# Kernel tuning notes

Measured on AMD Instinct MI355X. Metric: run time of the kernel, lower is better.

## Reference

```python
import jax, jax.numpy as jnp
import numpy as np

N, E = 50000, 800000
NODE_DIM, EDGE_DIM, TIME_DIM, OUT_DIM, N_HEADS = 128, 64, 16, 128, 4
IN_DIM = NODE_DIM + EDGE_DIM + TIME_DIM  # msg_proj input


def setup_inputs() -> dict:
    key = jax.random.key(0)
    ks = jax.random.split(key, 8)
    x = jax.random.normal(ks[0], (N, NODE_DIM), dtype=jnp.float32)
    edge_index = jax.random.randint(ks[1], (2, E), 0, N, dtype=jnp.int32)
    edge_feat = jax.random.normal(ks[2], (E, EDGE_DIM), dtype=jnp.float32)
    time_deltas = jax.random.uniform(ks[3], (E,), dtype=jnp.float32)
    # parameters
    gammas = jnp.ones((TIME_DIM,), jnp.float32)  # ExponentialTimeDecay init_gamma=1.0
    Wm = 0.02 * jax.random.normal(ks[4], (IN_DIM, OUT_DIM), dtype=jnp.float32)
    bm = jnp.zeros((OUT_DIM,), jnp.float32)
    Wa = 0.02 * jax.random.normal(ks[5], (2 * OUT_DIM, N_HEADS), dtype=jnp.float32)
    ba = jnp.zeros((N_HEADS,), jnp.float32)
    Wo = 0.02 * jax.random.normal(ks[6], (OUT_DIM + NODE_DIM, OUT_DIM), dtype=jnp.float32)
    bo = jnp.zeros((OUT_DIM,), jnp.float32)
    ln_g = jnp.ones((OUT_DIM,), jnp.float32)
    ln_b = jnp.zeros((OUT_DIM,), jnp.float32)
    return {"x": x, "edge_index": edge_index, "edge_feat": edge_feat,
            "time_deltas": time_deltas, "gammas": gammas, "Wm": Wm, "bm": bm,
            "Wa": Wa, "ba": ba, "Wo": Wo, "bo": bo, "ln_g": ln_g, "ln_b": ln_b}


def reference(x, edge_index, edge_feat, time_deltas, gammas, Wm, bm, Wa, ba, Wo, bo, ln_g, ln_b):
    src, dst = edge_index[0], edge_index[1]
    # exponential time decay encoding: (E, TIME_DIM)
    dt = jnp.clip(time_deltas, 0.0)[:, None]
    time_enc = jnp.exp(-jax.nn.softplus(gammas)[None, :] * dt)
    # gather + project messages: (E, OUT_DIM)
    msg_in = jnp.concatenate([x[src], edge_feat, time_enc], axis=-1)
    msgs = msg_in @ Wm + bm
    # edge attention, softmax over ALL edges (dim=0, as in the torch code)
    attn_in = jnp.concatenate([msgs, x[dst]], axis=-1)  # (E, 2*OUT_DIM)
    attn_logits = attn_in @ Wa + ba                      # (E, N_HEADS)
    attn_weight = jnp.mean(jax.nn.softmax(attn_logits, axis=0), axis=-1, keepdims=True)
    weighted = msgs * attn_weight
    # scatter-add into per-node aggregates: (N, OUT_DIM)
    agg = jax.ops.segment_sum(weighted, dst, num_segments=N)
    # output MLP (dropout is identity in eval) + LayerNorm
    out = jax.nn.gelu(jnp.concatenate([agg, x], axis=-1) @ Wo + bo, approximate=False)
    mu = jnp.mean(out, axis=-1, keepdims=True)
    var = jnp.mean((out - mu) ** 2, axis=-1, keepdims=True)
    return (out - mu) / jnp.sqrt(var + 1e-5) * ln_g + ln_b
```

## Files before the change

kernel.cpp:

```cpp
#include <hip/hip_runtime.h>
#include <math.h>

#define N_NODES 50000
#define N_EDGES 800000
#define ND 128
#define ED 64
#define TD 16
#define OD 128
#define NH 4
#define INDIM 208
#define K2DIM 336
#define KPAD 352
#define WTPITCH 360
#define NPAD 50048

#define OFF_A      0ll
#define OFF_EINFO  8808448ll
#define OFF_RANK   12008448ll
#define OFF_DENOM  12808448ll
#define OFF_SPG    12808464ll
#define OFF_WFUSE  12808480ll
#define OFF_BFUSE  12809312ll
#define OFF_BMO    12809328ll
#define OFF_XS4    12809456ll
#define OFF_XD4    13009456ll
#define OFF_CNT    13209456ll
#define OFF_START  13259456ll
#define OFF_SW     13309472ll
#define OFF_WT     13359520ll
#define OFF_EFC    13382560ll
#define OFF_XBF    38982560ll
#define WS_FLOATS  42182560ll

typedef __attribute__((ext_vector_type(8))) short short8v;
typedef __attribute__((ext_vector_type(4))) float f32x4;

__device__ inline unsigned short f2bf(float f) {
  unsigned u = __float_as_uint(f);
  unsigned r = (u + 0x7fffu + ((u >> 16) & 1u)) >> 16;
  return (unsigned short)r;
}
__device__ inline float bf2f(unsigned us) {
  return __uint_as_float(us << 16);
}

__global__ void k0_prep(const float* __restrict__ Wm, const float* __restrict__ bm,
                        const float* __restrict__ Wa, const float* __restrict__ ba,
                        const float* __restrict__ Wo, const float* __restrict__ gammas,
                        float* __restrict__ ws) {
  int b = blockIdx.x, j = threadIdx.x;
  unsigned short* Wt = (unsigned short*)(ws + OFF_WT);
  if (b < INDIM) {
    float acc = 0.f;
    for (int m = 0; m < OD; ++m) acc += Wm[b * OD + m] * Wo[m * OD + j];
    Wt[j * WTPITCH + b] = f2bf(acc);
    if (j < NH) {
      float a = 0.f;
      for (int m = 0; m < OD; ++m) a += Wm[b * OD + m] * Wa[m * NH + j];
      ws[OFF_WFUSE + (long)b * NH + j] = a;
    }
  } else if (b < K2DIM) {
    Wt[j * WTPITCH + b] = f2bf(Wo[(OD + b - INDIM) * OD + j]);
  } else {
    if (j < TD) ws[OFF_SPG + j] = log1pf(expf(gammas[j]));
    if (j < NH) {
      float a = ba[j];
      for (int m = 0; m < OD; ++m) a += bm[m] * Wa[m * NH + j];
      ws[OFF_BFUSE + j] = a;
    }
    float a2 = 0.f;
    for (int m = 0; m < OD; ++m) a2 += bm[m] * Wo[m * OD + j];
    ws[OFF_BMO + j] = a2;
    for (int p = K2DIM; p < KPAD; ++p) Wt[j * WTPITCH + p] = 0;
  }
}

__global__ __launch_bounds__(256) void k0b_nodeproj(
    const float* __restrict__ x, const float* __restrict__ Wa,
    float* __restrict__ ws) {
  __shared__ float wf[ND * NH];
  __shared__ float wab[ND * NH];
  int tid = threadIdx.x;
  for (int i = tid; i < ND * NH; i += 256) { wf[i] = ws[OFF_WFUSE + i]; wab[i] = Wa[ND * NH + i]; }
  __syncthreads();
  int lane = tid & 63, wv = tid >> 6;
  long n = (long)blockIdx.x * 4 + wv;
  if (n >= N_NODES) return;
  float v0 = x[n * ND + lane], v1 = x[n * ND + 64 + lane];
  unsigned short* xbf = (unsigned short*)(ws + OFF_XBF);
  xbf[n * ND + lane] = f2bf(v0);
  xbf[n * ND + 64 + lane] = f2bf(v1);
  float s0, s1, s2, s3, d0, d1, d2, d3;
  s0 = v0 * wf[lane * 4 + 0] + v1 * wf[(64 + lane) * 4 + 0];
  s1 = v0 * wf[lane * 4 + 1] + v1 * wf[(64 + lane) * 4 + 1];
  s2 = v0 * wf[lane * 4 + 2] + v1 * wf[(64 + lane) * 4 + 2];
  s3 = v0 * wf[lane * 4 + 3] + v1 * wf[(64 + lane) * 4 + 3];
  d0 = v0 * wab[lane * 4 + 0] + v1 * wab[(64 + lane) * 4 + 0];
  d1 = v0 * wab[lane * 4 + 1] + v1 * wab[(64 + lane) * 4 + 1];
  d2 = v0 * wab[lane * 4 + 2] + v1 * wab[(64 + lane) * 4 + 2];
  d3 = v0 * wab[lane * 4 + 3] + v1 * wab[(64 + lane) * 4 + 3];
  for (int off = 32; off; off >>= 1) {
    s0 += __shfl_xor(s0, off); s1 += __shfl_xor(s1, off);
    s2 += __shfl_xor(s2, off); s3 += __shfl_xor(s3, off);
    d0 += __shfl_xor(d0, off); d1 += __shfl_xor(d1, off);
    d2 += __shfl_xor(d2, off); d3 += __shfl_xor(d3, off);
  }
  if (lane == 0) {
    reinterpret_cast<float4*>(ws + OFF_XS4)[n] = make_float4(s0, s1, s2, s3);
    reinterpret_cast<float4*>(ws + OFF_XD4)[n] = make_float4(d0, d1, d2, d3);
  }
}

__global__ __launch_bounds__(256) void k_count(const int* __restrict__ ei,
                                               float* __restrict__ ws) {
  int* cnt = reinterpret_cast<int*>(ws + OFF_CNT);
  int* rank = reinterpret_cast<int*>(ws + OFF_RANK);
  for (long e = (long)blockIdx.x * 256 + threadIdx.x; e < N_EDGES;
       e += (long)gridDim.x * 256)
    rank[e] = atomicAdd(&cnt[ei[N_EDGES + e]], 1);
}

__global__ __launch_bounds__(1024) void k_scan(float* __restrict__ ws) {
  const int* cnt = reinterpret_cast<const int*>(ws + OFF_CNT);
  int* startp = reinterpret_cast<int*>(ws + OFF_START);
  __shared__ int wsum[16];
  int tid = threadIdx.x;
  int lo = tid * 49, hi = min(lo + 49, N_NODES);
  int s = 0;
  for (int i = lo; i < hi; ++i) s += cnt[i];
  int lane = tid & 63, wv = tid >> 6;
  int sc = s;
  for (int off = 1; off < 64; off <<= 1) {
    int t = __shfl_up(sc, off);
    if (lane >= off) sc += t;
  }
  if (lane == 63) wsum[wv] = sc;
  __syncthreads();
  if (tid == 0) {
    int run = 0;
    for (int i = 0; i < 16; ++i) { int t = wsum[i]; wsum[i] = run; run += t; }
  }
  __syncthreads();
  int run = wsum[wv] + sc - s;
  for (int i = lo; i < hi; ++i) { startp[i] = run; run += cnt[i]; }
  if (tid == 1023) startp[N_NODES] = run;
}

__global__ __launch_bounds__(256) void k1c(
    const int* __restrict__ ei, const float* __restrict__ ef,
    const float* __restrict__ td, float* __restrict__ ws) {
  __shared__ float wef[ED * NH];
  __shared__ float wte[TD * NH];
  __shared__ float bf[NH];
  __shared__ float spg[TD];
  __shared__ float part[NH];
  int tid = threadIdx.x;
  for (int i = tid; i < ED * NH; i += 256) wef[i] = ws[OFF_WFUSE + ND * NH + i];
  if (tid < TD * NH) wte[tid] = ws[OFF_WFUSE + (ND + ED) * NH + tid];
  if (tid < NH) { bf[tid] = ws[OFF_BFUSE + tid]; part[tid] = 0.f; }
  if (tid < TD) spg[tid] = ws[OFF_SPG + tid];
  __syncthreads();

  int lane = tid & 63;
  int q = lane >> 4, r = lane & 15, h = r & 3;
  long wid = ((long)blockIdx.x * 256 + tid) >> 6;
  long stride = (long)gridDim.x * 16;
  const float4* ef4 = reinterpret_cast<const float4*>(ef);
  const float* xsf = ws + OFF_XS4;
  const float* xdf = ws + OFF_XD4;
  const int* rank = reinterpret_cast<const int*>(ws + OFF_RANK);
  const int* startp = reinterpret_cast<const int*>(ws + OFF_START);
  uint2* efc2 = reinterpret_cast<uint2*>(ws + OFF_EFC);
  uint4* einfoC = reinterpret_cast<uint4*>(ws + OFF_EINFO);

  float wr[16];
#pragma unroll
  for (int i = 0; i < 16; ++i) wr[i] = wef[16 * r + i];
  float spg_r = spg[r];
  float wt0 = wte[r * 4 + 0], wt1 = wte[r * 4 + 1];
  float wt2 = wte[r * 4 + 2], wt3 = wte[r * 4 + 3];
  float bfh = bf[h];
  float p = 0.f;
  int base16 = lane & 48;

  for (long e = wid * 4 + q; e < N_EDGES; e += stride) {
    int s = ei[e];
    int d = ei[N_EDGES + e];
    float dt = fmaxf(td[e], 0.f);
    int pos = startp[d] + rank[e];
    float4 efv = ef4[e * 16 + r];
    float ls = xsf[4l * s + h];
    float ld = xdf[4l * d + h];
    float te = __expf(-spg_r * dt);
    uint2 eb;
    eb.x = (unsigned)f2bf(efv.x) | ((unsigned)f2bf(efv.y) << 16);
    eb.y = (unsigned)f2bf(efv.z) | ((unsigned)f2bf(efv.w) << 16);
    efc2[(long)pos * 16 + r] = eb;
    float a0 = efv.x * wr[0] + efv.y * wr[4] + efv.z * wr[8]  + efv.w * wr[12] + te * wt0;
    float a1 = efv.x * wr[1] + efv.y * wr[5] + efv.z * wr[9]  + efv.w * wr[13] + te * wt1;
    float a2 = efv.x * wr[2] + efv.y * wr[6] + efv.z * wr[10] + efv.w * wr[14] + te * wt2;
    float a3 = efv.x * wr[3] + efv.y * wr[7] + efv.z * wr[11] + efv.w * wr[15] + te * wt3;
    a0 += __shfl_xor(a0, 1); a1 += __shfl_xor(a1, 1);
    a2 += __shfl_xor(a2, 1); a3 += __shfl_xor(a3, 1);
    a0 += __shfl_xor(a0, 2); a1 += __shfl_xor(a1, 2);
    a2 += __shfl_xor(a2, 2); a3 += __shfl_xor(a3, 2);
    float v = a0;
    v = (h == 1) ? a1 : v;
    v = (h == 2) ? a2 : v;
    v = (h == 3) ? a3 : v;
    v += __shfl_xor(v, 4);
    v += __shfl_xor(v, 8);
    float ev = __expf(v + ls + ld + bfh);
    if (r < 4) p += ev;
    float e0 = __shfl(ev, base16 + 0), e1 = __shfl(ev, base16 + 1);
    float e2 = __shfl(ev, base16 + 2), e3 = __shfl(ev, base16 + 3);
    if (r == 0) {
      unsigned dt16 = (unsigned)(dt * 65535.f + 0.5f);
      if (dt16 > 65535u) dt16 = 65535u;
      uint4 pk;
      pk.x = (unsigned)s | (dt16 << 16);
      pk.y = (unsigned)f2bf(e0) | ((unsigned)f2bf(e1) << 16);
      pk.z = (unsigned)f2bf(e2) | ((unsigned)f2bf(e3) << 16);
      pk.w = 0u;
      einfoC[pos] = pk;
    }
  }
  p += __shfl_xor(p, 16);
  p += __shfl_xor(p, 32);
  if (lane < 4) atomicAdd(&part[lane], p);
  __syncthreads();
  if (tid < NH) atomicAdd(&ws[OFF_DENOM + tid], part[tid]);
}

__global__ __launch_bounds__(256) void k4a_agg(float* __restrict__ ws) {
  __shared__ float spg_s[TD];
  __shared__ float invs[NH];
  int tid = threadIdx.x;
  if (tid < TD) spg_s[tid] = ws[OFF_SPG + tid];
  if (tid < NH) invs[tid] = 0.25f / ws[OFF_DENOM + tid];
  __syncthreads();
  int lane = tid & 63;
  long wid = (long)blockIdx.x * 4 + (tid >> 6);
  long nw = (long)gridDim.x * 4;
  const int* start = reinterpret_cast<const int*>(ws + OFF_START);
  const uint4* einfoC = reinterpret_cast<const uint4*>(ws + OFF_EINFO);
  unsigned short* A = (unsigned short*)(ws + OFF_A);
  const unsigned short* xbf = (const unsigned short*)(ws + OFF_XBF);
  const unsigned short* efc = (const unsigned short*)(ws + OFF_EFC);
  float spg_l = spg_s[lane & 15];
  float inv0 = invs[0], inv1 = invs[1], inv2 = invs[2], inv3 = invs[3];

  for (long n = wid; n < N_NODES; n += nw) {
    int i0 = start[n], i1 = start[n + 1];
    float a0 = 0.f, a1 = 0.f, a2 = 0.f, a3 = 0.f, asw = 0.f;
    for (int base = i0; base < i1; base += 64) {
      int m = min(64, i1 - base);
      uint4 pk = make_uint4(0u, 0u, 0u, 0u);
      if (lane < m) pk = einfoC[base + lane];
      int j = 0;
      for (; j + 4 <= m; j += 4) {
        unsigned xu[4], zu[4], wu[4];
#pragma unroll
        for (int u = 0; u < 4; ++u) {
          xu[u] = (unsigned)__shfl((int)pk.x, j + u);
          zu[u] = (unsigned)__shfl((int)pk.y, j + u);
          wu[u] = (unsigned)__shfl((int)pk.z, j + u);
        }
        unsigned xa[4], xb[4], ec[4];
#pragma unroll
        for (int u = 0; u < 4; ++u) {
          int s = (int)(xu[u] & 0xffffu);
          xa[u] = xbf[(long)s * ND + lane];
          xb[u] = xbf[(long)s * ND + 64 + lane];
          ec[u] = efc[(long)(base + j + u) * ED + lane];
        }
#pragma unroll
        for (int u = 0; u < 4; ++u) {
          float w = bf2f(zu[u] & 0xffffu) * inv0 + bf2f(zu[u] >> 16) * inv1 +
                    bf2f(wu[u] & 0xffffu) * inv2 + bf2f(wu[u] >> 16) * inv3;
          float dt = (float)(xu[u] >> 16) * (1.f / 65535.f);
          a0 += w * bf2f(xa[u]);
          a1 += w * bf2f(xb[u]);
          a2 += w * bf2f(ec[u]);
          a3 += w * __expf(-spg_l * dt);
          asw += w;
        }
      }
      for (; j < m; ++j) {
        unsigned xu = (unsigned)__shfl((int)pk.x, j);
        unsigned zu = (unsigned)__shfl((int)pk.y, j);
        unsigned wu = (unsigned)__shfl((int)pk.z, j);
        int s = (int)(xu & 0xffffu);
        float w = bf2f(zu & 0xffffu) * inv0 + bf2f(zu >> 16) * inv1 +
                  bf2f(wu & 0xffffu) * inv2 + bf2f(wu >> 16) * inv3;
        float dt = (float)(xu >> 16) * (1.f / 65535.f);
        a0 += w * bf2f(xbf[(long)s * ND + lane]);
        a1 += w * bf2f(xbf[(long)s * ND + 64 + lane]);
        a2 += w * bf2f(efc[(long)(base + j) * ED + lane]);
        a3 += w * __expf(-spg_l * dt);
        asw += w;
      }
    }
    unsigned short* Ar = A + n * KPAD;
    Ar[lane] = f2bf(a0);
    Ar[64 + lane] = f2bf(a1);
    Ar[128 + lane] = f2bf(a2);
    if (lane < TD) Ar[192 + lane] = f2bf(a3);
    Ar[INDIM + lane] = xbf[n * ND + lane];
    Ar[INDIM + 64 + lane] = xbf[n * ND + 64 + lane];
    if (lane < 16) Ar[K2DIM + lane] = 0;
    if (lane == 0) ws[OFF_SW + n] = asw;
  }
}

__global__ __launch_bounds__(256) void k4b_mlp(
    const float* __restrict__ bo, const float* __restrict__ lng,
    const float* __restrict__ lnb, const float* __restrict__ ws,
    float* __restrict__ out) {
  __shared__ unsigned short wt[128 * WTPITCH];
  __shared__ float tbl[512];
  int tid = threadIdx.x;
  {
    const unsigned* wg = (const unsigned*)(ws + OFF_WT);
    unsigned* wl = (unsigned*)wt;
    for (int i = tid; i < 128 * WTPITCH / 2; i += 256) wl[i] = wg[i];
    if (tid < 128) {
      tbl[tid] = bo[tid];
      tbl[128 + tid] = ws[OFF_BMO + tid];
      tbl[256 + tid] = lng[tid];
      tbl[384 + tid] = lnb[tid];
    }
  }
  __syncthreads();

  int lane = tid & 63, wv = tid >> 6;
  int c0 = lane & 15, grp = lane >> 4;
  long n0 = (long)blockIdx.x * 64 + (long)wv * 16;
  const unsigned short* A = (const unsigned short*)(ws + OFF_A);
  const unsigned short* Arow = A + (n0 + c0) * KPAD;

  f32x4 acc[8];
#pragma unroll
  for (int t = 0; t < 8; ++t) acc[t] = (f32x4){0.f, 0.f, 0.f, 0.f};

#pragma unroll
  for (int kt = 0; kt < 11; ++kt) {
    short8v afrag = *reinterpret_cast<const short8v*>(Arow + kt * 32 + grp * 8);
#pragma unroll
    for (int t = 0; t < 8; ++t) {
      short8v bfrag = *reinterpret_cast<const short8v*>(&wt[(t * 16 + c0) * WTPITCH + kt * 32 + grp * 8]);
      acc[t] = __builtin_amdgcn_mfma_f32_16x16x32_bf16(afrag, bfrag, acc[t], 0, 0, 0);
    }
  }

  const float* swp = ws + OFF_SW;
  float res[4][8];
#pragma unroll
  for (int r = 0; r < 4; ++r) {
    long row = n0 + grp * 4 + r;
    float sw = swp[row];
    float s = 0.f, s2 = 0.f;
#pragma unroll
    for (int t = 0; t < 8; ++t) {
      int col = c0 + 16 * t;
      float a = acc[t][r] + tbl[col] + sw * tbl[128 + col];
      float h = 0.5f * a * (1.f + erff(a * 0.70710678118654752f));
      res[r][t] = h;
      s += h; s2 += h * h;
    }
    s += __shfl_xor(s, 1);  s2 += __shfl_xor(s2, 1);
    s += __shfl_xor(s, 2);  s2 += __shfl_xor(s2, 2);
    s += __shfl_xor(s, 4);  s2 += __shfl_xor(s2, 4);
    s += __shfl_xor(s, 8);  s2 += __shfl_xor(s2, 8);
    float mu = s * (1.f / 128.f);
    float var = s2 * (1.f / 128.f) - mu * mu;
    float rstd = rsqrtf(var + 1e-5f);
    if (row < N_NODES) {
      float* op = out + row * OD;
#pragma unroll
      for (int t = 0; t < 8; ++t) {
        int col = c0 + 16 * t;
        op[col] = (res[r][t] - mu) * rstd * tbl[256 + col] + tbl[384 + col];
      }
    }
  }
}

extern "C" void kernel_launch(void* const* d_in, const int* in_sizes, int n_in,
                              void* d_out, int out_size, void* d_ws, size_t ws_size,
                              hipStream_t stream) {
  const float* x   = (const float*)d_in[0];
  const int*   ei  = (const int*)d_in[1];
  const float* ef  = (const float*)d_in[2];
  const float* td  = (const float*)d_in[3];
  const float* gm  = (const float*)d_in[4];
  const float* Wm  = (const float*)d_in[5];
  const float* bm  = (const float*)d_in[6];
  const float* Wa  = (const float*)d_in[7];
  const float* ba  = (const float*)d_in[8];
  const float* Wo  = (const float*)d_in[9];
  const float* bo  = (const float*)d_in[10];
  const float* lng = (const float*)d_in[11];
  const float* lnb = (const float*)d_in[12];
  float* ws = (float*)d_ws;
  float* out = (float*)d_out;
  if (ws_size < (size_t)WS_FLOATS * 4) return;

  hipMemsetAsync(ws + OFF_CNT, 0, 50000 * 4, stream);
  hipMemsetAsync(ws + OFF_DENOM, 0, 64, stream);

  k0_prep<<<K2DIM + 1, 128, 0, stream>>>(Wm, bm, Wa, ba, Wo, gm, ws);
  k0b_nodeproj<<<12500, 256, 0, stream>>>(x, Wa, ws);
  k_count<<<2048, 256, 0, stream>>>(ei, ws);
  k_scan<<<1, 1024, 0, stream>>>(ws);
  k1c<<<2048, 256, 0, stream>>>(ei, ef, td, ws);
  k4a_agg<<<2048, 256, 0, stream>>>(ws);
  k4b_mlp<<<(NPAD / 64), 256, 0, stream>>>(bo, lng, lnb, ws, out);
}
```

Before: 412.8 us.

## Remap edge-logit lanes per head and stage edge info in LDS

In the edge pass, each lane now computes a 16-feature partial dot product for a single head, which removes most of the cross-lane shuffle reduction and the per-head select. The bf16 edge-feature copy is now written with wider 16-byte stores by one lane per group. The packed edge-info record is reorganised so that each of four lanes writes its own 32-bit word holding one head's exp value, with the source index and quantised dt packed into the upper halves. The aggregation kernel stages each 64-edge chunk of these records in per-wave LDS and reads them back as uint4, replacing the broadcast shuffles. The trade-off is redundant float4 loads across the four head lanes and four exps per lane instead of one.

```diff
diff --git a/kernel.cpp b/kernel.cpp
--- a/kernel.cpp
+++ b/kernel.cpp
@@ -152,17 +152,17 @@
   __shared__ float wef[ED * NH];
   __shared__ float wte[TD * NH];
   __shared__ float bf[NH];
-  __shared__ float spg[TD];
+  __shared__ float spgs[TD];
   __shared__ float part[NH];
   int tid = threadIdx.x;
   for (int i = tid; i < ED * NH; i += 256) wef[i] = ws[OFF_WFUSE + ND * NH + i];
   if (tid < TD * NH) wte[tid] = ws[OFF_WFUSE + (ND + ED) * NH + tid];
   if (tid < NH) { bf[tid] = ws[OFF_BFUSE + tid]; part[tid] = 0.f; }
-  if (tid < TD) spg[tid] = ws[OFF_SPG + tid];
+  if (tid < TD) spgs[tid] = ws[OFF_SPG + tid];
   __syncthreads();
 
   int lane = tid & 63;
-  int q = lane >> 4, r = lane & 15, h = r & 3;
+  int q = lane >> 4, r = lane & 15, h = r & 3, c = r >> 2;
   long wid = ((long)blockIdx.x * 256 + tid) >> 6;
   long stride = (long)gridDim.x * 16;
   const float4* ef4 = reinterpret_cast<const float4*>(ef);
@@ -170,59 +170,59 @@
   const float* xdf = ws + OFF_XD4;
   const int* rank = reinterpret_cast<const int*>(ws + OFF_RANK);
   const int* startp = reinterpret_cast<const int*>(ws + OFF_START);
-  uint2* efc2 = reinterpret_cast<uint2*>(ws + OFF_EFC);
-  uint4* einfoC = reinterpret_cast<uint4*>(ws + OFF_EINFO);
-
-  float wr[16];
-#pragma unroll
-  for (int i = 0; i < 16; ++i) wr[i] = wef[16 * r + i];
-  float spg_r = spg[r];
-  float wt0 = wte[r * 4 + 0], wt1 = wte[r * 4 + 1];
-  float wt2 = wte[r * 4 + 2], wt3 = wte[r * 4 + 3];
+  uint4* efc4 = reinterpret_cast<uint4*>(ws + OFF_EFC);
+  unsigned* einfoU = reinterpret_cast<unsigned*>(ws + OFF_EINFO);
+
+  float wk[16];
+#pragma unroll
+  for (int i = 0; i < 16; ++i) wk[i] = wef[(16 * c + i) * 4 + h];
+  float wt4[4], sp4[4];
+#pragma unroll
+  for (int i = 0; i < 4; ++i) { wt4[i] = wte[(4 * c + i) * 4 + h]; sp4[i] = spgs[4 * c + i]; }
   float bfh = bf[h];
   float p = 0.f;
-  int base16 = lane & 48;
 
   for (long e = wid * 4 + q; e < N_EDGES; e += stride) {
     int s = ei[e];
     int d = ei[N_EDGES + e];
     float dt = fmaxf(td[e], 0.f);
     int pos = startp[d] + rank[e];
-    float4 efv = ef4[e * 16 + r];
-    float ls = xsf[4l * s + h];
-    float ld = xdf[4l * d + h];
-    float te = __expf(-spg_r * dt);
-    uint2 eb;
-    eb.x = (unsigned)f2bf(efv.x) | ((unsigned)f2bf(efv.y) << 16);
-    eb.y = (unsigned)f2bf(efv.z) | ((unsigned)f2bf(efv.w) << 16);
-    efc2[(long)pos * 16 + r] = eb;
-    float a0 = efv.x * wr[0] + efv.y * wr[4] + efv.z * wr[8]  + efv.w * wr[12] + te * wt0;
-    float a1 = efv.x * wr[1] + efv.y * wr[5] + efv.z * wr[9]  + efv.w * wr[13] + te * wt1;
-    float a2 = efv.x * wr[2] + efv.y * wr[6] + efv.z * wr[10] + efv.w * wr[14] + te * wt2;
-    float a3 = efv.x * wr[3] + efv.y * wr[7] + efv.z * wr[11] + efv.w * wr[15] + te * wt3;
-    a0 += __shfl_xor(a0, 1); a1 += __shfl_xor(a1, 1);
-    a2 += __shfl_xor(a2, 1); a3 += __shfl_xor(a3, 1);
-    a0 += __shfl_xor(a0, 2); a1 += __shfl_xor(a1, 2);
-    a2 += __shfl_xor(a2, 2); a3 += __shfl_xor(a3, 2);
-    float v = a0;
-    v = (h == 1) ? a1 : v;
-    v = (h == 2) ? a2 : v;
-    v = (h == 3) ? a3 : v;
-    v += __shfl_xor(v, 4);
-    v += __shfl_xor(v, 8);
-    float ev = __expf(v + ls + ld + bfh);
-    if (r < 4) p += ev;
-    float e0 = __shfl(ev, base16 + 0), e1 = __shfl(ev, base16 + 1);
-    float e2 = __shfl(ev, base16 + 2), e3 = __shfl(ev, base16 + 3);
-    if (r == 0) {
+    float4 v0 = ef4[e * 16 + 4 * c + 0];
+    float4 v1 = ef4[e * 16 + 4 * c + 1];
+    float4 v2 = ef4[e * 16 + 4 * c + 2];
+    float4 v3 = ef4[e * 16 + 4 * c + 3];
+    if (h == 0) {
+      uint4 o0, o1;
+      o0.x = (unsigned)f2bf(v0.x) | ((unsigned)f2bf(v0.y) << 16);
+      o0.y = (unsigned)f2bf(v0.z) | ((unsigned)f2bf(v0.w) << 16);
+      o0.z = (unsigned)f2bf(v1.x) | ((unsigned)f2bf(v1.y) << 16);
+      o0.w = (unsigned)f2bf(v1.z) | ((unsigned)f2bf(v1.w) << 16);
+      o1.x = (unsigned)f2bf(v2.x) | ((unsigned)f2bf(v2.y) << 16);
+      o1.y = (unsigned)f2bf(v2.z) | ((unsigned)f2bf(v2.w) << 16);
+      o1.z = (unsigned)f2bf(v3.x) | ((unsigned)f2bf(v3.y) << 16);
+      o1.w = (unsigned)f2bf(v3.z) | ((unsigned)f2bf(v3.w) << 16);
+      efc4[(long)pos * 8 + 2 * c + 0] = o0;
+      efc4[(long)pos * 8 + 2 * c + 1] = o1;
+    }
+    float a;
+    a  = v0.x * wk[0]  + v0.y * wk[1]  + v0.z * wk[2]  + v0.w * wk[3];
+    a += v1.x * wk[4]  + v1.y * wk[5]  + v1.z * wk[6]  + v1.w * wk[7];
+    a += v2.x * wk[8]  + v2.y * wk[9]  + v2.z * wk[10] + v2.w * wk[11];
+    a += v3.x * wk[12] + v3.y * wk[13] + v3.z * wk[14] + v3.w * wk[15];
+    float te0 = __expf(-sp4[0] * dt), te1 = __expf(-sp4[1] * dt);
+    float te2 = __expf(-sp4[2] * dt), te3 = __expf(-sp4[3] * dt);
+    a += te0 * wt4[0] + te1 * wt4[1] + te2 * wt4[2] + te3 * wt4[3];
+    a += __shfl_xor(a, 4);
+    a += __shfl_xor(a, 8);
+    float ev = __expf(a + xsf[4l * s + h] + xdf[4l * d + h] + bfh);
+    if (r < 4) {
+      p += ev;
       unsigned dt16 = (unsigned)(dt * 65535.f + 0.5f);
       if (dt16 > 65535u) dt16 = 65535u;
-      uint4 pk;
-      pk.x = (unsigned)s | (dt16 << 16);
-      pk.y = (unsigned)f2bf(e0) | ((unsigned)f2bf(e1) << 16);
-      pk.z = (unsigned)f2bf(e2) | ((unsigned)f2bf(e3) << 16);
-      pk.w = 0u;
-      einfoC[pos] = pk;
+      unsigned wrd = (unsigned)f2bf(ev);
+      if (r == 0) wrd |= ((unsigned)s << 16);
+      if (r == 1) wrd |= (dt16 << 16);
+      einfoU[(long)pos * 4 + r] = wrd;
     }
   }
   p += __shfl_xor(p, 16);
@@ -235,12 +235,14 @@
 __global__ __launch_bounds__(256) void k4a_agg(float* __restrict__ ws) {
   __shared__ float spg_s[TD];
   __shared__ float invs[NH];
+  __shared__ uint4 st[4][64];
   int tid = threadIdx.x;
   if (tid < TD) spg_s[tid] = ws[OFF_SPG + tid];
   if (tid < NH) invs[tid] = 0.25f / ws[OFF_DENOM + tid];
   __syncthreads();
   int lane = tid & 63;
-  long wid = (long)blockIdx.x * 4 + (tid >> 6);
+  int wv = tid >> 6;
+  long wid = (long)blockIdx.x * 4 + wv;
   long nw = (long)gridDim.x * 4;
   const int* start = reinterpret_cast<const int*>(ws + OFF_START);
   const uint4* einfoC = reinterpret_cast<const uint4*>(ws + OFF_EINFO);
@@ -255,30 +257,29 @@
     float a0 = 0.f, a1 = 0.f, a2 = 0.f, a3 = 0.f, asw = 0.f;
     for (int base = i0; base < i1; base += 64) {
       int m = min(64, i1 - base);
-      uint4 pk = make_uint4(0u, 0u, 0u, 0u);
-      if (lane < m) pk = einfoC[base + lane];
+      if (lane < m) st[wv][lane] = einfoC[base + lane];
       int j = 0;
       for (; j + 4 <= m; j += 4) {
-        unsigned xu[4], zu[4], wu[4];
+        uint4 q0 = st[wv][j + 0], q1 = st[wv][j + 1];
+        uint4 q2 = st[wv][j + 2], q3 = st[wv][j + 3];
+        unsigned xa[4], xb[4], ec[4];
+        int s0i = (int)(q0.x >> 16), s1i = (int)(q1.x >> 16);
+        int s2i = (int)(q2.x >> 16), s3i = (int)(q3.x >> 16);
+        xa[0] = xbf[(long)s0i * ND + lane]; xb[0] = xbf[(long)s0i * ND + 64 + lane];
+        xa[1] = xbf[(long)s1i * ND + lane]; xb[1] = xbf[(long)s1i * ND + 64 + lane];
+        xa[2] = xbf[(long)s2i * ND + lane]; xb[2] = xbf[(long)s2i * ND + 64 + lane];
+        xa[3] = xbf[(long)s3i * ND + lane]; xb[3] = xbf[(long)s3i * ND + 64 + lane];
+        ec[0] = efc[(long)(base + j + 0) * ED + lane];
+        ec[1] = efc[(long)(base + j + 1) * ED + lane];
+        ec[2] = efc[(long)(base + j + 2) * ED + lane];
+        ec[3] = efc[(long)(base + j + 3) * ED + lane];
+        uint4 qs[4] = {q0, q1, q2, q3};
 #pragma unroll
         for (int u = 0; u < 4; ++u) {
-          xu[u] = (unsigned)__shfl((int)pk.x, j + u);
-          zu[u] = (unsigned)__shfl((int)pk.y, j + u);
-          wu[u] = (unsigned)__shfl((int)pk.z, j + u);
-        }
-        unsigned xa[4], xb[4], ec[4];
-#pragma unroll
-        for (int u = 0; u < 4; ++u) {
-          int s = (int)(xu[u] & 0xffffu);
-          xa[u] = xbf[(long)s * ND + lane];
-          xb[u] = xbf[(long)s * ND + 64 + lane];
-          ec[u] = efc[(long)(base + j + u) * ED + lane];
-        }
-#pragma unroll
-        for (int u = 0; u < 4; ++u) {
-          float w = bf2f(zu[u] & 0xffffu) * inv0 + bf2f(zu[u] >> 16) * inv1 +
-                    bf2f(wu[u] & 0xffffu) * inv2 + bf2f(wu[u] >> 16) * inv3;
-          float dt = (float)(xu[u] >> 16) * (1.f / 65535.f);
+          uint4 qq = qs[u];
+          float w = bf2f(qq.x & 0xffffu) * inv0 + bf2f(qq.y & 0xffffu) * inv1 +
+                    bf2f(qq.z & 0xffffu) * inv2 + bf2f(qq.w & 0xffffu) * inv3;
+          float dt = (float)(qq.y >> 16) * (1.f / 65535.f);
           a0 += w * bf2f(xa[u]);
           a1 += w * bf2f(xb[u]);
           a2 += w * bf2f(ec[u]);
@@ -287,15 +288,13 @@
         }
       }
       for (; j < m; ++j) {
-        unsigned xu = (unsigned)__shfl((int)pk.x, j);
-        unsigned zu = (unsigned)__shfl((int)pk.y, j);
-        unsigned wu = (unsigned)__shfl((int)pk.z, j);
-        int s = (int)(xu & 0xffffu);
-        float w = bf2f(zu & 0xffffu) * inv0 + bf2f(zu >> 16) * inv1 +
-                  bf2f(wu & 0xffffu) * inv2 + bf2f(wu >> 16) * inv3;
-        float dt = (float)(xu >> 16) * (1.f / 65535.f);
-        a0 += w * bf2f(xbf[(long)s * ND + lane]);
-        a1 += w * bf2f(xbf[(long)s * ND + 64 + lane]);
+        uint4 qq = st[wv][j];
+        int si = (int)(qq.x >> 16);
+        float w = bf2f(qq.x & 0xffffu) * inv0 + bf2f(qq.y & 0xffffu) * inv1 +
+                  bf2f(qq.z & 0xffffu) * inv2 + bf2f(qq.w & 0xffffu) * inv3;
+        float dt = (float)(qq.y >> 16) * (1.f / 65535.f);
+        a0 += w * bf2f(xbf[(long)si * ND + lane]);
+        a1 += w * bf2f(xbf[(long)si * ND + 64 + lane]);
         a2 += w * bf2f(efc[(long)(base + j) * ED + lane]);
         a3 += w * __expf(-spg_l * dt);
         asw += w;
```

New measurement: 481.0 us. 1.17x slower.
